# Kernel optimization log

Hardware: AMD Instinct MI355X
Metric: run time of the kernel (lower is better)

Reference implementation:

```python
import jax, jax.numpy as jnp
import numpy as np

NUM_CODES = 1024
CODE_DIM = 256
EMA_DECAY = 0.99
EPSILON = 1e-05
SOFTMAX_TEMP = 0.1


def setup_inputs() -> dict:
    key = jax.random.key(0)
    k1, k2, k3 = jax.random.split(key, 3)
    z = jax.random.normal(k1, (32, 1024, CODE_DIM), dtype=jnp.float32)
    embed = jax.random.normal(k2, (NUM_CODES, CODE_DIM), dtype=jnp.float32) * 0.1
    cluster_size = jnp.ones((NUM_CODES,), dtype=jnp.float32)
    embed_avg = jax.random.normal(k3, (NUM_CODES, CODE_DIM), dtype=jnp.float32) * 0.1
    return {"z": z, "embed": embed, "cluster_size": cluster_size, "embed_avg": embed_avg}


def reference(z, embed, cluster_size, embed_avg):
    orig_shape = z.shape
    flat_z = z.reshape(-1, CODE_DIM)                      # [N, D]
    N = flat_z.shape[0]

    # squared euclidean distances: [N, K]
    dist = (jnp.sum(flat_z * flat_z, axis=1, keepdims=True)
            - 2.0 * jnp.einsum('nd,kd->nk', flat_z, embed)
            + jnp.sum(embed * embed, axis=1)[None, :])

    codes = jnp.argmin(dist, axis=1)                      # [N]
    z_q = embed[codes]                                    # [N, D]
    soft_assign = jax.nn.softmax(-dist / SOFTMAX_TEMP, axis=-1)

    # EMA updates (training branch), functional: return new buffers
    counts = jax.ops.segment_sum(jnp.ones((N,), dtype=flat_z.dtype), codes,
                                 num_segments=NUM_CODES)            # encodings.sum(0)
    embed_sum = jax.ops.segment_sum(flat_z, codes, num_segments=NUM_CODES)  # [K, D]
    new_cluster_size = EMA_DECAY * cluster_size + (1.0 - EMA_DECAY) * counts
    new_embed_avg = EMA_DECAY * embed_avg + (1.0 - EMA_DECAY) * embed_sum
    n = jnp.sum(new_cluster_size)
    cs_norm = (new_cluster_size + EPSILON) / (n + NUM_CODES * EPSILON) * n
    new_embed = new_embed_avg / cs_norm[:, None]

    commitment_loss = jnp.mean((flat_z - jax.lax.stop_gradient(z_q)) ** 2)

    # straight-through estimator
    z_q_st = (flat_z + jax.lax.stop_gradient(z_q - flat_z)).reshape(orig_shape)
    codes_out = codes.reshape(orig_shape[:-1])

    avg_probs = counts / N
    log_p = jnp.log(avg_probs + 1e-10)
    code_entropy = -jnp.sum(avg_probs * log_p)
    perplexity = jnp.exp(code_entropy)

    soft_assign_out = soft_assign.reshape(*orig_shape[:-1], NUM_CODES)
    return (z_q_st, codes_out, commitment_loss, perplexity, code_entropy,
            soft_assign_out, new_embed, new_cluster_size, new_embed_avg)
```

## Files before the change

### kernel.cpp

```cpp
#include <hip/hip_runtime.h>
#include <math.h>

#define N_ROWS 32768
#define DIM 256
#define K_CODES 1024

#define WS_LOSS   0
#define WS_NSUM   1024
#define WS_ZZ     2048
#define WS_EE     34816
#define WS_COUNTS 35840
#define WS_ESUM   36864
#define WS_TOTAL  (36864 + K_CODES * DIM)

#define OFF_ZQ    0ull
#define OFF_CODES 8388608ull
#define OFF_LOSS  8421376ull
#define OFF_PERP  8421377ull
#define OFF_ENT   8421378ull
#define OFF_SOFT  8421379ull
#define OFF_NEMB  41975811ull
#define OFF_NCS   42237955ull
#define OFF_NEA   42238979ull

#define OFF_EPACK 41975812ull
#define PLANE_Z   8388608ull
#define PLANE_E   262144ull


typedef __attribute__((ext_vector_type(8))) short bf16x8;
typedef __attribute__((ext_vector_type(4))) float f32x4;

__device__ __forceinline__ ushort f2bf(float x) {
    union { float f; unsigned u; } a; a.f = x;
    unsigned r = a.u + 0x7fffu + ((a.u >> 16) & 1u);
    return (ushort)(r >> 16);
}
__device__ __forceinline__ float bf2f(ushort h) {
    union { unsigned u; float f; } a; a.u = ((unsigned)h) << 16;
    return a.f;
}

__global__ __launch_bounds__(256) void k0_zero(float* ws) {
    int i = blockIdx.x * 256 + threadIdx.x;
    if (i < WS_TOTAL) ws[i] = 0.0f;
}

__global__ __launch_bounds__(256) void k1_norms(const float* __restrict__ z,
                                                const float* __restrict__ embed,
                                                float* __restrict__ ws,
                                                float* out) {
    ushort* zhi = (ushort*)(out + OFF_ZQ);
    ushort* zlo = zhi + PLANE_Z;
    ushort* ehi = (ushort*)(out + OFF_EPACK);
    ushort* elo = ehi + PLANE_E;

    int wave = threadIdx.x >> 6;
    int lane = threadIdx.x & 63;
    int row = blockIdx.x * 4 + wave;
    const float* src = (row < N_ROWS) ? (z + (size_t)row * DIM)
                                      : (embed + (size_t)(row - N_ROWS) * DIM);
    float4 v = *(const float4*)(src + lane * 4);
    float s = v.x * v.x + v.y * v.y + v.z * v.z + v.w * v.w;

    ushort h0 = f2bf(v.x), h1 = f2bf(v.y), h2 = f2bf(v.z), h3 = f2bf(v.w);
    ushort l0 = f2bf(v.x - bf2f(h0)), l1 = f2bf(v.y - bf2f(h1));
    ushort l2 = f2bf(v.z - bf2f(h2)), l3 = f2bf(v.w - bf2f(h3));
    unsigned hA = (unsigned)h0 | ((unsigned)h1 << 16);
    unsigned hB = (unsigned)h2 | ((unsigned)h3 << 16);
    unsigned lA = (unsigned)l0 | ((unsigned)l1 << 16);
    unsigned lB = (unsigned)l2 | ((unsigned)l3 << 16);

    int r = (row < N_ROWS) ? row : (row - N_ROWS);
    int kb = lane >> 3;
    int lg = (lane >> 1) & 3;
    int j0 = (lane & 1) * 4;
    size_t idx = ((size_t)(r >> 4) * 8 + kb) * 512
               + (size_t)(lg * 16 + (r & 15)) * 8 + j0;

    if (row < N_ROWS) {
        *(uint2*)(zhi + idx) = make_uint2(hA, hB);
        *(uint2*)(zlo + idx) = make_uint2(lA, lB);
    } else {
        *(uint2*)(ehi + idx) = make_uint2(hA, hB);
        *(uint2*)(elo + idx) = make_uint2(lA, lB);
    }

    #pragma unroll
    for (int off = 32; off; off >>= 1) s += __shfl_down(s, off, 64);
    if (lane == 0) {
        if (row < N_ROWS) ws[WS_ZZ + row] = s;
        else              ws[WS_EE + (row - N_ROWS)] = s;
    }
}

__global__ __launch_bounds__(256, 3) void k2_mfma(const float* __restrict__ ws,
                                                  float* out) {
    const ushort* zhi = (const ushort*)(out + OFF_ZQ);
    const ushort* ehi = (const ushort*)(out + OFF_EPACK);

    int tid  = threadIdx.x;
    int lane = tid & 63;
    int wid  = tid >> 6;
    int wr   = wid >> 1, wc = wid & 1;
    int rowBase = blockIdx.y * 64 + wr * 32;
    int colBase = blockIdx.x * 256 + wc * 128;
    int l15 = lane & 15, lg = lane >> 4;

    f32x4 acc[2][8];
    #pragma unroll
    for (int fi = 0; fi < 2; ++fi)
        #pragma unroll
        for (int fj = 0; fj < 8; ++fj)
            acc[fi][fj] = (f32x4){0.f, 0.f, 0.f, 0.f};

    int rowBlk = rowBase >> 4;
    int colBlk = colBase >> 4;

    for (int kb = 0; kb < 8; ++kb) {
        bf16x8 ah[2], al[2];
        #pragma unroll
        for (int fi = 0; fi < 2; ++fi) {
            const ushort* pa = zhi + ((size_t)(rowBlk + fi) * 8 + kb) * 512 + lane * 8;
            ah[fi] = *(const bf16x8*)pa;
            al[fi] = *(const bf16x8*)(pa + PLANE_Z);
        }
        #pragma unroll
        for (int fj = 0; fj < 8; ++fj) {
            const ushort* pb = ehi + ((size_t)(colBlk + fj) * 8 + kb) * 512 + lane * 8;
            bf16x8 bh = *(const bf16x8*)pb;
            bf16x8 bl = *(const bf16x8*)(pb + PLANE_E);
            #pragma unroll
            for (int fi = 0; fi < 2; ++fi) {
                acc[fi][fj] = __builtin_amdgcn_mfma_f32_16x16x32_bf16(ah[fi], bh, acc[fi][fj], 0, 0, 0);
                acc[fi][fj] = __builtin_amdgcn_mfma_f32_16x16x32_bf16(ah[fi], bl, acc[fi][fj], 0, 0, 0);
                acc[fi][fj] = __builtin_amdgcn_mfma_f32_16x16x32_bf16(al[fi], bh, acc[fi][fj], 0, 0, 0);
            }
        }
    }

    #pragma unroll
    for (int fi = 0; fi < 2; ++fi) {
        #pragma unroll
        for (int q = 0; q < 4; ++q) {
            int n = rowBase + fi * 16 + lg * 4 + q;
            float zzn = ws[WS_ZZ + n];
            float* orow = out + OFF_SOFT + (size_t)n * K_CODES;
            #pragma unroll
            for (int fj = 0; fj < 8; ++fj) {
                int k = colBase + fj * 16 + l15;
                orow[k] = (zzn - 2.0f * acc[fi][fj][q]) + ws[WS_EE + k];
            }
        }
    }
}

__device__ inline void blockMinIdx(float& v, int& idx, float* smv, int* smi) {
    int lane = threadIdx.x & 63, wave = threadIdx.x >> 6;
    #pragma unroll
    for (int off = 32; off; off >>= 1) {
        float ov = __shfl_down(v, off, 64);
        int   oi = __shfl_down(idx, off, 64);
        if (ov < v || (ov == v && oi < idx)) { v = ov; idx = oi; }
    }
    if (lane == 0) { smv[wave] = v; smi[wave] = idx; }
    __syncthreads();
    v = smv[0]; idx = smi[0];
    #pragma unroll
    for (int w = 1; w < 4; ++w) {
        float ov = smv[w]; int oi = smi[w];
        if (ov < v || (ov == v && oi < idx)) { v = ov; idx = oi; }
    }
    __syncthreads();
}

__device__ inline float blockSum(float v, float* sm) {
    int lane = threadIdx.x & 63, wave = threadIdx.x >> 6;
    #pragma unroll
    for (int off = 32; off; off >>= 1) v += __shfl_down(v, off, 64);
    if (lane == 0) sm[wave] = v;
    __syncthreads();
    float r = sm[0] + sm[1] + sm[2] + sm[3];
    __syncthreads();
    return r;
}

__global__ __launch_bounds__(256) void k3_softmax(const float* __restrict__ z,
                                                  const float* __restrict__ embed,
                                                  float* __restrict__ ws,
                                                  float* __restrict__ out) {
    __shared__ float smv[4];
    __shared__ int   smi[4];
    __shared__ float sms[4];
    __shared__ double sdd[4];
    __shared__ int cand[8];
    __shared__ int ncand;

    int n = blockIdx.x;
    int tid = threadIdx.x;
    float* dptr = out + OFF_SOFT + (size_t)n * K_CODES;

    float d[4];
    float lmin = 3.4e38f; int lidx = 0;
    #pragma unroll
    for (int j = 0; j < 4; ++j) {
        int k = tid + 256 * j;
        d[j] = dptr[k];
        if (d[j] < lmin) { lmin = d[j]; lidx = k; }
    }
    float bmin = lmin; int code = lidx;
    blockMinIdx(bmin, code, smv, smi);

    if (tid == 0) ncand = 0;
    __syncthreads();
    #pragma unroll
    for (int j = 0; j < 4; ++j) {
        if (d[j] <= bmin + 1e-3f) {
            int slot = atomicAdd(&ncand, 1);
            if (slot < 8) cand[slot] = tid + 256 * j;
        }
    }
    __syncthreads();
    int nc = ncand;
    float zv = z[(size_t)n * DIM + tid];
    if (nc > 1) {
        int lim = nc < 8 ? nc : 8;
        float zzn = ws[WS_ZZ + n];
        float bestd = 0.f; int bestk = -1;
        for (int c = 0; c < lim; ++c) {
            int kc = cand[c];
            double part = (double)zv * (double)embed[(size_t)kc * DIM + tid];
            int lane = tid & 63, wave = tid >> 6;
            #pragma unroll
            for (int off = 32; off; off >>= 1) part += __shfl_down(part, off, 64);
            if (lane == 0) sdd[wave] = part;
            __syncthreads();
            double dot = sdd[0] + sdd[1] + sdd[2] + sdd[3];
            __syncthreads();
            float d32 = (zzn - 2.0f * (float)dot) + ws[WS_EE + kc];
            if (bestk < 0 || d32 < bestd || (d32 == bestd && kc < bestk)) { bestd = d32; bestk = kc; }
        }
        code = bestk;
    }

    float p[4]; float s = 0.f;
    #pragma unroll
    for (int j = 0; j < 4; ++j) { p[j] = __expf((bmin - d[j]) * 10.0f); s += p[j]; }
    float tot = blockSum(s, sms);
    float inv = 1.0f / tot;
    #pragma unroll
    for (int j = 0; j < 4; ++j) dptr[tid + 256 * j] = p[j] * inv;

    float qv = embed[(size_t)code * DIM + tid];
    out[OFF_ZQ + (size_t)n * DIM + tid] = qv;
    float diff = zv - qv;
    float lsum = blockSum(diff * diff, sms);
    atomicAdd(&ws[WS_ESUM + (size_t)code * DIM + tid], zv);
    if (tid == 0) {
        atomicAdd(&ws[WS_LOSS + (n & 1023)], lsum);
        atomicAdd(&ws[WS_COUNTS + code], 1.0f);
        out[OFF_CODES + n] = (float)code;
    }
}

__global__ __launch_bounds__(1024) void k4a_stats(const float* __restrict__ cluster_size,
                                                  float* __restrict__ ws,
                                                  float* __restrict__ out) {
    __shared__ float sm[16];
    int k = threadIdx.x;
    int lane = k & 63, wave = k >> 6;
    float cnt = ws[WS_COUNTS + k];
    float ncs = 0.99f * cluster_size[k] + 0.01f * cnt;
    out[OFF_NCS + k] = ncs;

    float v = ncs;
    #pragma unroll
    for (int off = 32; off; off >>= 1) v += __shfl_down(v, off, 64);
    if (lane == 0) sm[wave] = v;
    __syncthreads();
    if (k == 0) {
        float t = 0.f;
        for (int w = 0; w < 16; ++w) t += sm[w];
        ws[WS_NSUM] = t;
    }
    __syncthreads();

    float avg = cnt / (float)N_ROWS;
    v = -avg * logf(avg + 1e-10f);
    #pragma unroll
    for (int off = 32; off; off >>= 1) v += __shfl_down(v, off, 64);
    if (lane == 0) sm[wave] = v;
    __syncthreads();
    if (k == 0) {
        float ent = 0.f;
        for (int w = 0; w < 16; ++w) ent += sm[w];
        out[OFF_ENT]  = ent;
        out[OFF_PERP] = expf(ent);
    }
    __syncthreads();

    v = ws[WS_LOSS + k];
    #pragma unroll
    for (int off = 32; off; off >>= 1) v += __shfl_down(v, off, 64);
    if (lane == 0) sm[wave] = v;
    __syncthreads();
    if (k == 0) {
        float t = 0.f;
        for (int w = 0; w < 16; ++w) t += sm[w];
        out[OFF_LOSS] = t / 8388608.0f;
    }
}

__global__ __launch_bounds__(256) void k4b_embed(const float* __restrict__ embed_avg,
                                                 const float* __restrict__ ws,
                                                 float* __restrict__ out) {
    int k = blockIdx.x, d = threadIdx.x;
    float es  = ws[WS_ESUM + (size_t)k * DIM + d];
    float nea = 0.99f * embed_avg[(size_t)k * DIM + d] + 0.01f * es;
    out[OFF_NEA + (size_t)k * DIM + d] = nea;
    float ncs  = out[OFF_NCS + k];
    float nsum = ws[WS_NSUM];
    float csn  = (ncs + 1e-5f) / (nsum + K_CODES * 1e-5f) * nsum;
    out[OFF_NEMB + (size_t)k * DIM + d] = nea / csn;
}

extern "C" void kernel_launch(void* const* d_in, const int* in_sizes, int n_in,
                              void* d_out, int out_size, void* d_ws, size_t ws_size,
                              hipStream_t stream) {
    const float* z            = (const float*)d_in[0];
    const float* embed        = (const float*)d_in[1];
    const float* cluster_size = (const float*)d_in[2];
    const float* embed_avg    = (const float*)d_in[3];
    float* out = (float*)d_out;
    float* ws  = (float*)d_ws;

    k0_zero<<<(WS_TOTAL + 255) / 256, 256, 0, stream>>>(ws);
    k1_norms<<<(N_ROWS + K_CODES) / 4, 256, 0, stream>>>(z, embed, ws, out);
    k2_mfma<<<dim3(K_CODES / 256, N_ROWS / 64), 256, 0, stream>>>(ws, out);
    k3_softmax<<<N_ROWS, 256, 0, stream>>>(z, embed, ws, out);
    k4a_stats<<<1, 1024, 0, stream>>>(cluster_size, ws, out);
    k4b_embed<<<K_CODES, 256, 0, stream>>>(embed_avg, ws, out);
}
```

Baseline: 369.4 us.

## Fuse distance GEMM with argmin, softmax and EMA scatter per row block

The MFMA distance kernel now has each block cover 32 full rows across all 1024 codes. Argmin, tie refinement, softmax normalisation and the scatter accumulations run in the same kernel's epilogue, so the distance matrix is never written to and re-read from global memory. The z_q gather moves to a small separate kernel, because the packed z planes alias the z_q output region. In exchange there are more registers per thread (16 accumulator tiles), less parallelism per row tile, and a serial block-wide tie-refinement loop.

```diff
diff --git a/kernel.cpp b/kernel.cpp
--- a/kernel.cpp
+++ b/kernel.cpp
@@ -94,173 +94,209 @@
     }
 }
 
-__global__ __launch_bounds__(256, 3) void k2_mfma(const float* __restrict__ ws,
-                                                  float* out) {
+__global__ __launch_bounds__(512, 2) void k2_fused(const float* __restrict__ z,
+                                                   const float* __restrict__ embed,
+                                                   float* __restrict__ ws,
+                                                   float* __restrict__ out) {
+    __shared__ float wmin[8][16];
+    __shared__ int   widx[8][16];
+    __shared__ float wsum[8][16];
+    __shared__ float rowmin_s[32];
+    __shared__ int   rowcode_s[32];
+    __shared__ float rowinv_s[32];
+    __shared__ int   rownc[32];
+    __shared__ int   rowcand[32][8];
+    __shared__ double sdd[8];
+    __shared__ int   anytie;
+
     const ushort* zhi = (const ushort*)(out + OFF_ZQ);
     const ushort* ehi = (const ushort*)(out + OFF_EPACK);
 
     int tid  = threadIdx.x;
     int lane = tid & 63;
     int wid  = tid >> 6;
-    int wr   = wid >> 1, wc = wid & 1;
-    int rowBase = blockIdx.y * 64 + wr * 32;
-    int colBase = blockIdx.x * 256 + wc * 128;
+    int wr   = wid >> 2, wc = wid & 3;
+    int rowBase = blockIdx.x * 32;
     int l15 = lane & 15, lg = lane >> 4;
 
-    f32x4 acc[2][8];
-    #pragma unroll
-    for (int fi = 0; fi < 2; ++fi)
-        #pragma unroll
-        for (int fj = 0; fj < 8; ++fj)
-            acc[fi][fj] = (f32x4){0.f, 0.f, 0.f, 0.f};
-
-    int rowBlk = rowBase >> 4;
-    int colBlk = colBase >> 4;
+    f32x4 acc[16];
+    #pragma unroll
+    for (int fj = 0; fj < 16; ++fj) acc[fj] = (f32x4){0.f, 0.f, 0.f, 0.f};
+
+    int rowBlk = blockIdx.x * 2 + wr;
+    int colBlk = wc * 16;
 
     for (int kb = 0; kb < 8; ++kb) {
-        bf16x8 ah[2], al[2];
-        #pragma unroll
-        for (int fi = 0; fi < 2; ++fi) {
-            const ushort* pa = zhi + ((size_t)(rowBlk + fi) * 8 + kb) * 512 + lane * 8;
-            ah[fi] = *(const bf16x8*)pa;
-            al[fi] = *(const bf16x8*)(pa + PLANE_Z);
-        }
-        #pragma unroll
-        for (int fj = 0; fj < 8; ++fj) {
+        const ushort* pa = zhi + ((size_t)rowBlk * 8 + kb) * 512 + lane * 8;
+        bf16x8 ah = *(const bf16x8*)pa;
+        bf16x8 al = *(const bf16x8*)(pa + PLANE_Z);
+        #pragma unroll
+        for (int fj = 0; fj < 16; ++fj) {
             const ushort* pb = ehi + ((size_t)(colBlk + fj) * 8 + kb) * 512 + lane * 8;
             bf16x8 bh = *(const bf16x8*)pb;
             bf16x8 bl = *(const bf16x8*)(pb + PLANE_E);
-            #pragma unroll
-            for (int fi = 0; fi < 2; ++fi) {
-                acc[fi][fj] = __builtin_amdgcn_mfma_f32_16x16x32_bf16(ah[fi], bh, acc[fi][fj], 0, 0, 0);
-                acc[fi][fj] = __builtin_amdgcn_mfma_f32_16x16x32_bf16(ah[fi], bl, acc[fi][fj], 0, 0, 0);
-                acc[fi][fj] = __builtin_amdgcn_mfma_f32_16x16x32_bf16(al[fi], bh, acc[fi][fj], 0, 0, 0);
+            acc[fj] = __builtin_amdgcn_mfma_f32_16x16x32_bf16(ah, bh, acc[fj], 0, 0, 0);
+            acc[fj] = __builtin_amdgcn_mfma_f32_16x16x32_bf16(ah, bl, acc[fj], 0, 0, 0);
+            acc[fj] = __builtin_amdgcn_mfma_f32_16x16x32_bf16(al, bh, acc[fj], 0, 0, 0);
+        }
+    }
+
+    #pragma unroll
+    for (int q = 0; q < 4; ++q) {
+        float zzn = ws[WS_ZZ + rowBase + wr * 16 + lg * 4 + q];
+        #pragma unroll
+        for (int fj = 0; fj < 16; ++fj) {
+            float eek = ws[WS_EE + wc * 256 + fj * 16 + l15];
+            acc[fj][q] = (zzn - 2.0f * acc[fj][q]) + eek;
+        }
+    }
+
+    #pragma unroll
+    for (int q = 0; q < 4; ++q) {
+        float bm = acc[0][q]; int bi = wc * 256 + l15;
+        #pragma unroll
+        for (int fj = 1; fj < 16; ++fj) {
+            if (acc[fj][q] < bm) { bm = acc[fj][q]; bi = wc * 256 + fj * 16 + l15; }
+        }
+        #pragma unroll
+        for (int m = 1; m <= 8; m <<= 1) {
+            float ov = __shfl_xor(bm, m, 64);
+            int   oi = __shfl_xor(bi, m, 64);
+            if (ov < bm || (ov == bm && oi < bi)) { bm = ov; bi = oi; }
+        }
+        if (l15 == 0) {
+            wmin[wid][lg * 4 + q] = bm;
+            widx[wid][lg * 4 + q] = bi;
+        }
+    }
+    if (tid == 0) anytie = 0;
+    if (tid < 32) rownc[tid] = 0;
+    __syncthreads();
+    if (tid < 32) {
+        int rw = tid >> 4, rl = tid & 15;
+        float bv = wmin[rw * 4][rl]; int bi = widx[rw * 4][rl];
+        #pragma unroll
+        for (int w = 1; w < 4; ++w) {
+            float ov = wmin[rw * 4 + w][rl]; int oi = widx[rw * 4 + w][rl];
+            if (ov < bv || (ov == bv && oi < bi)) { bv = ov; bi = oi; }
+        }
+        rowmin_s[tid] = bv; rowcode_s[tid] = bi;
+    }
+    __syncthreads();
+
+    float mrow[4];
+    #pragma unroll
+    for (int q = 0; q < 4; ++q) mrow[q] = rowmin_s[wr * 16 + lg * 4 + q];
+
+    #pragma unroll
+    for (int q = 0; q < 4; ++q) {
+        int r = wr * 16 + lg * 4 + q;
+        float thr = mrow[q] + 1e-3f;
+        #pragma unroll
+        for (int fj = 0; fj < 16; ++fj) {
+            if (acc[fj][q] <= thr) {
+                int slot = atomicAdd(&rownc[r], 1);
+                if (slot < 8) rowcand[r][slot] = wc * 256 + fj * 16 + l15;
             }
         }
     }
-
-    #pragma unroll
-    for (int fi = 0; fi < 2; ++fi) {
-        #pragma unroll
-        for (int q = 0; q < 4; ++q) {
-            int n = rowBase + fi * 16 + lg * 4 + q;
+    __syncthreads();
+    if (tid < 32 && rownc[tid] > 1) atomicAdd(&anytie, 1);
+    __syncthreads();
+    if (anytie) {
+        for (int r = 0; r < 32; ++r) {
+            int nc = rownc[r];
+            if (nc <= 1) continue;
+            int lim = nc < 8 ? nc : 8;
+            int n = rowBase + r;
             float zzn = ws[WS_ZZ + n];
-            float* orow = out + OFF_SOFT + (size_t)n * K_CODES;
-            #pragma unroll
-            for (int fj = 0; fj < 8; ++fj) {
-                int k = colBase + fj * 16 + l15;
-                orow[k] = (zzn - 2.0f * acc[fi][fj][q]) + ws[WS_EE + k];
+            float bestd = 0.f; int bestk = -1;
+            for (int ci = 0; ci < lim; ++ci) {
+                int kc = rowcand[r][ci];
+                double part = 0.0;
+                if (tid < 256)
+                    part = (double)z[(size_t)n * DIM + tid] * (double)embed[(size_t)kc * DIM + tid];
+                #pragma unroll
+                for (int off = 32; off; off >>= 1) part += __shfl_down(part, off, 64);
+                if (lane == 0) sdd[wid] = part;
+                __syncthreads();
+                double dot = 0.0;
+                for (int w = 0; w < 8; ++w) dot += sdd[w];
+                float d32 = (zzn - 2.0f * (float)dot) + ws[WS_EE + kc];
+                if (bestk < 0 || d32 < bestd || (d32 == bestd && kc < bestk)) { bestd = d32; bestk = kc; }
+                __syncthreads();
             }
-        }
-    }
-}
-
-__device__ inline void blockMinIdx(float& v, int& idx, float* smv, int* smi) {
-    int lane = threadIdx.x & 63, wave = threadIdx.x >> 6;
-    #pragma unroll
-    for (int off = 32; off; off >>= 1) {
-        float ov = __shfl_down(v, off, 64);
-        int   oi = __shfl_down(idx, off, 64);
-        if (ov < v || (ov == v && oi < idx)) { v = ov; idx = oi; }
-    }
-    if (lane == 0) { smv[wave] = v; smi[wave] = idx; }
-    __syncthreads();
-    v = smv[0]; idx = smi[0];
-    #pragma unroll
-    for (int w = 1; w < 4; ++w) {
-        float ov = smv[w]; int oi = smi[w];
-        if (ov < v || (ov == v && oi < idx)) { v = ov; idx = oi; }
-    }
-    __syncthreads();
-}
-
-__device__ inline float blockSum(float v, float* sm) {
-    int lane = threadIdx.x & 63, wave = threadIdx.x >> 6;
-    #pragma unroll
-    for (int off = 32; off; off >>= 1) v += __shfl_down(v, off, 64);
-    if (lane == 0) sm[wave] = v;
-    __syncthreads();
-    float r = sm[0] + sm[1] + sm[2] + sm[3];
-    __syncthreads();
-    return r;
-}
-
-__global__ __launch_bounds__(256) void k3_softmax(const float* __restrict__ z,
-                                                  const float* __restrict__ embed,
-                                                  float* __restrict__ ws,
-                                                  float* __restrict__ out) {
-    __shared__ float smv[4];
-    __shared__ int   smi[4];
-    __shared__ float sms[4];
-    __shared__ double sdd[4];
-    __shared__ int cand[8];
-    __shared__ int ncand;
-
-    int n = blockIdx.x;
-    int tid = threadIdx.x;
-    float* dptr = out + OFF_SOFT + (size_t)n * K_CODES;
-
-    float d[4];
-    float lmin = 3.4e38f; int lidx = 0;
-    #pragma unroll
-    for (int j = 0; j < 4; ++j) {
-        int k = tid + 256 * j;
-        d[j] = dptr[k];
-        if (d[j] < lmin) { lmin = d[j]; lidx = k; }
-    }
-    float bmin = lmin; int code = lidx;
-    blockMinIdx(bmin, code, smv, smi);
-
-    if (tid == 0) ncand = 0;
-    __syncthreads();
-    #pragma unroll
-    for (int j = 0; j < 4; ++j) {
-        if (d[j] <= bmin + 1e-3f) {
-            int slot = atomicAdd(&ncand, 1);
-            if (slot < 8) cand[slot] = tid + 256 * j;
-        }
-    }
-    __syncthreads();
-    int nc = ncand;
-    float zv = z[(size_t)n * DIM + tid];
-    if (nc > 1) {
-        int lim = nc < 8 ? nc : 8;
-        float zzn = ws[WS_ZZ + n];
-        float bestd = 0.f; int bestk = -1;
-        for (int c = 0; c < lim; ++c) {
-            int kc = cand[c];
-            double part = (double)zv * (double)embed[(size_t)kc * DIM + tid];
-            int lane = tid & 63, wave = tid >> 6;
-            #pragma unroll
-            for (int off = 32; off; off >>= 1) part += __shfl_down(part, off, 64);
-            if (lane == 0) sdd[wave] = part;
-            __syncthreads();
-            double dot = sdd[0] + sdd[1] + sdd[2] + sdd[3];
-            __syncthreads();
-            float d32 = (zzn - 2.0f * (float)dot) + ws[WS_EE + kc];
-            if (bestk < 0 || d32 < bestd || (d32 == bestd && kc < bestk)) { bestd = d32; bestk = kc; }
-        }
-        code = bestk;
-    }
-
-    float p[4]; float s = 0.f;
-    #pragma unroll
-    for (int j = 0; j < 4; ++j) { p[j] = __expf((bmin - d[j]) * 10.0f); s += p[j]; }
-    float tot = blockSum(s, sms);
-    float inv = 1.0f / tot;
-    #pragma unroll
-    for (int j = 0; j < 4; ++j) dptr[tid + 256 * j] = p[j] * inv;
-
-    float qv = embed[(size_t)code * DIM + tid];
-    out[OFF_ZQ + (size_t)n * DIM + tid] = qv;
-    float diff = zv - qv;
-    float lsum = blockSum(diff * diff, sms);
-    atomicAdd(&ws[WS_ESUM + (size_t)code * DIM + tid], zv);
-    if (tid == 0) {
-        atomicAdd(&ws[WS_LOSS + (n & 1023)], lsum);
-        atomicAdd(&ws[WS_COUNTS + code], 1.0f);
-        out[OFF_CODES + n] = (float)code;
-    }
+            if (tid == 0) rowcode_s[r] = bestk;
+        }
+        __syncthreads();
+    }
+
+    #pragma unroll
+    for (int q = 0; q < 4; ++q) {
+        float m = mrow[q];
+        float s = 0.f;
+        #pragma unroll
+        for (int fj = 0; fj < 16; ++fj) {
+            acc[fj][q] = __expf((m - acc[fj][q]) * 10.0f);
+            s += acc[fj][q];
+        }
+        #pragma unroll
+        for (int mk = 1; mk <= 8; mk <<= 1) s += __shfl_xor(s, mk, 64);
+        if (l15 == 0) wsum[wid][lg * 4 + q] = s;
+    }
+    __syncthreads();
+    if (tid < 32) {
+        int rw = tid >> 4, rl = tid & 15;
+        float t = wsum[rw * 4][rl] + wsum[rw * 4 + 1][rl]
+                + wsum[rw * 4 + 2][rl] + wsum[rw * 4 + 3][rl];
+        rowinv_s[tid] = 1.0f / t;
+    }
+    __syncthreads();
+    #pragma unroll
+    for (int q = 0; q < 4; ++q) {
+        int n = rowBase + wr * 16 + lg * 4 + q;
+        float inv = rowinv_s[wr * 16 + lg * 4 + q];
+        float* orow = out + OFF_SOFT + (size_t)n * K_CODES;
+        #pragma unroll
+        for (int fj = 0; fj < 16; ++fj)
+            orow[wc * 256 + fj * 16 + l15] = acc[fj][q] * inv;
+    }
+
+    {
+        int r   = tid >> 4;
+        int seg = tid & 15;
+        int n = rowBase + r;
+        int code = rowcode_s[r];
+        int dd = seg * 16;
+        float lsum = 0.f;
+        #pragma unroll
+        for (int qq = 0; qq < 4; ++qq) {
+            float4 e4 = *(const float4*)&embed[(size_t)code * DIM + dd + qq * 4];
+            float4 z4 = *(const float4*)&z[(size_t)n * DIM + dd + qq * 4];
+            float dx = z4.x - e4.x, dy = z4.y - e4.y, dz_ = z4.z - e4.z, dw = z4.w - e4.w;
+            lsum += dx * dx + dy * dy + dz_ * dz_ + dw * dw;
+            atomicAdd(&ws[WS_ESUM + (size_t)code * DIM + dd + qq * 4 + 0], z4.x);
+            atomicAdd(&ws[WS_ESUM + (size_t)code * DIM + dd + qq * 4 + 1], z4.y);
+            atomicAdd(&ws[WS_ESUM + (size_t)code * DIM + dd + qq * 4 + 2], z4.z);
+            atomicAdd(&ws[WS_ESUM + (size_t)code * DIM + dd + qq * 4 + 3], z4.w);
+        }
+        #pragma unroll
+        for (int off = 8; off; off >>= 1) lsum += __shfl_down(lsum, off, 16);
+        if (seg == 0) {
+            atomicAdd(&ws[WS_LOSS + (n & 1023)], lsum);
+            atomicAdd(&ws[WS_COUNTS + code], 1.0f);
+            out[OFF_CODES + n] = (float)code;
+        }
+    }
+}
+
+__global__ __launch_bounds__(256) void k3_zq(const float* __restrict__ embed,
+                                             float* __restrict__ out) {
+    int wave = threadIdx.x >> 6, lane = threadIdx.x & 63;
+    int n = blockIdx.x * 4 + wave;
+    int code = (int)out[OFF_CODES + n];
+    float4 e4 = *(const float4*)&embed[(size_t)code * DIM + lane * 4];
+    *(float4*)&out[OFF_ZQ + (size_t)n * DIM + lane * 4] = e4;
 }
 
 __global__ __launch_bounds__(1024) void k4a_stats(const float* __restrict__ cluster_size,
@@ -336,8 +372,8 @@
 
     k0_zero<<<(WS_TOTAL + 255) / 256, 256, 0, stream>>>(ws);
     k1_norms<<<(N_ROWS + K_CODES) / 4, 256, 0, stream>>>(z, embed, ws, out);
-    k2_mfma<<<dim3(K_CODES / 256, N_ROWS / 64), 256, 0, stream>>>(ws, out);
-    k3_softmax<<<N_ROWS, 256, 0, stream>>>(z, embed, ws, out);
+    k2_fused<<<N_ROWS / 32, 512, 0, stream>>>(z, embed, ws, out);
+    k3_zq<<<N_ROWS / 4, 256, 0, stream>>>(embed, out);
     k4a_stats<<<1, 1024, 0, stream>>>(cluster_size, ws, out);
     k4b_embed<<<K_CODES, 256, 0, stream>>>(embed_avg, ws, out);
 }
```

Result: slower. 734.6 us (+98.9%).
